# Kernel tuning notes

Hardware: AMD Instinct MI355X
Metric: run time of the kernel (lower is better)

Reference implementation:

```python
import jax, jax.numpy as jnp
import numpy as np

B, NH, N = 4, 4, 1000
NF = 256
TOPK = 10
ADJ_THRESH = 0.5
PSTEP = 3
BIG = 1e10


def construct_edges(s_cur, a_cur):
    """Top-k distance-based edge construction.
    s_cur: (B,N,3) positions, a_cur: (B,N) attributes; tool = a_cur > 0.5.
    Returns dense receiver/sender matrices Rr, Rs of shape (B, R=N*TOPK, N),
    padded with zero rows (equivalent to torch's contiguous packing).
    """
    b, n, _ = s_cur.shape
    tool = a_cur > 0.5  # mask is all-ones (no particle_nums)
    diff = s_cur[:, :, None, :] - s_cur[:, None, :, :]          # (B,N,N,3)
    dis = jnp.sum(diff * diff, axis=-1)                          # (B,N,N)
    # tool-tool pairs excluded (set huge distance)
    dis = jnp.where(tool[:, :, None] & tool[:, None, :], BIG, dis)
    neg_d, idx = jax.lax.top_k(-dis, TOPK)                       # smallest TOPK dists
    d = -neg_d                                                    # (B,N,TOPK)
    # edge valid if within threshold; receiver-is-tool edges zeroed
    # (connect_tools_all=False branch: adj[tool_mask_1 * mask_2] = 0)
    flag = (d < ADJ_THRESH * ADJ_THRESH) & (~tool[:, :, None])   # (B,N,TOPK)
    R = n * TOPK
    flagR = flag.reshape(b, R).astype(s_cur.dtype)
    send = idx.reshape(b, R)                                      # sender index per relation
    recv = jnp.repeat(jnp.arange(n), TOPK)                        # (R,) receiver index
    bi = jnp.arange(b)[:, None]
    ri = jnp.arange(R)[None, :]
    Rr = jnp.zeros((b, R, n), s_cur.dtype).at[bi, ri, recv[None, :]].set(flagR)
    Rs = jnp.zeros((b, R, n), s_cur.dtype).at[bi, ri, send].set(flagR)
    return Rr, Rs


def _forward(a_hist, s_hist, s_delta,
             pe_w0, pe_b0, pe_w1, pe_b1,
             re_w0, re_b0, re_w1, re_b1, re_w2, re_b2,
             rp_w, rp_b, pp_w, pp_b,
             pr_w0, pr_b0, pr_w1, pr_b1):
    relu = jax.nn.relu
    b, nh, n = a_hist.shape
    a = jnp.swapaxes(a_hist, 1, 2)                 # (B,N,NH)
    s = jnp.swapaxes(s_hist, 1, 2)                 # (B,N,NH,3)
    sd = jnp.swapaxes(s_delta, 1, 2).reshape(b, n, 3 * nh)  # (B,N,3*NH)
    a_cur = a[:, :, -1]                             # (B,N)
    s_cur = s[:, :, -1, :]                          # (B,N,3)

    Rr, Rs = construct_edges(s_cur, a_cur)          # (B,R,N)

    a_r = jnp.einsum('brn,bn->br', Rr, a_cur)[..., None]  # (B,R,1)
    a_s = jnp.einsum('brn,bn->br', Rs, a_cur)[..., None]
    s_r = jnp.einsum('brn,bnd->brd', Rr, s_cur)            # (B,R,3)
    s_s = jnp.einsum('brn,bnd->brd', Rs, s_cur)

    # particle encoder: Linear-ReLU-Linear-ReLU on cat[s_delta_flat, a_hist]
    pe_in = jnp.concatenate([sd, a], axis=2)               # (B,N,4*NH)
    particle_encode = relu(relu(pe_in @ pe_w0 + pe_b0) @ pe_w1 + pe_b1)

    re_in = jnp.concatenate([a_r, a_s, s_r - s_s], axis=2)
    h = relu(re_in @ re_w0 + re_b0)
    h = relu(h @ re_w1 + re_b1)
    relation_encode = relu(h @ re_w2 + re_b2)              # (B,R,NF)

    particle_effect = particle_encode
    for _ in range(PSTEP):
        eff_r = jnp.einsum('brn,bnd->brd', Rr, particle_effect)
        eff_s = jnp.einsum('brn,bnd->brd', Rs, particle_effect)
        effect_rel = relu(
            jnp.concatenate([relation_encode, eff_r, eff_s], axis=2) @ rp_w + rp_b)
        agg = jnp.einsum('brn,brd->bnd', Rr, effect_rel)   # Rr^T @ effect_rel
        particle_effect = relu(
            jnp.concatenate([particle_encode, agg], axis=2) @ pp_w + pp_b
            + particle_effect)

    pred = relu(particle_effect @ pr_w0 + pr_b0) @ pr_w1 + pr_b1  # (B,N,3)
    return pred + s_cur


def setup_inputs() -> dict:
    key = jax.random.key(0)
    ks = jax.random.split(key, 24)
    W = lambda k, shp: (jax.random.normal(k, shp, jnp.float32) * 0.05)
    inp = {
        'a_hist': jax.random.uniform(ks[0], (B, NH, N), jnp.float32),
        's_hist': jax.random.normal(ks[1], (B, NH, N, 3), jnp.float32),
        's_delta': jax.random.normal(ks[2], (B, NH, N, 3), jnp.float32),
        'pe_w0': W(ks[3], (4 * NH, NF)), 'pe_b0': W(ks[4], (NF,)),
        'pe_w1': W(ks[5], (NF, NF)),     'pe_b1': W(ks[6], (NF,)),
        're_w0': W(ks[7], (5, NF)),      're_b0': W(ks[8], (NF,)),
        're_w1': W(ks[9], (NF, NF)),     're_b1': W(ks[10], (NF,)),
        're_w2': W(ks[11], (NF, NF)),    're_b2': W(ks[12], (NF,)),
        'rp_w': W(ks[13], (3 * NF, NF)), 'rp_b': W(ks[14], (NF,)),
        'pp_w': W(ks[15], (2 * NF, NF)), 'pp_b': W(ks[16], (NF,)),
        'pr_w0': W(ks[17], (NF, NF)),    'pr_b0': W(ks[18], (NF,)),
        'pr_w1': W(ks[19], (NF, 3)),     'pr_b1': W(ks[20], (3,)),
    }
    return inp


def reference(a_hist, s_hist, s_delta,
              pe_w0, pe_b0, pe_w1, pe_b1,
              re_w0, re_b0, re_w1, re_b1, re_w2, re_b2,
              rp_w, rp_b, pp_w, pp_b,
              pr_w0, pr_b0, pr_w1, pr_b1):
    return _forward(a_hist, s_hist, s_delta,
                    pe_w0, pe_b0, pe_w1, pe_b1,
                    re_w0, re_b0, re_w1, re_b1, re_w2, re_b2,
                    rp_w, rp_b, pp_w, pp_b,
                    pr_w0, pr_b0, pr_w1, pr_b1)
```

## Files before the change

### kernel.cpp

```cpp
#include <hip/hip_runtime.h>
#include <hip/hip_bf16.h>

typedef unsigned short u16;
typedef unsigned int u32;

#define BATCH 4
#define NHIST 4
#define NPART 1000
#define NTOPK 10
#define NPT (BATCH*NPART)
#define NET (NPT*NTOPK)
#define EREG 5000
#define NRT 157

typedef __bf16 b8v __attribute__((ext_vector_type(8)));
typedef float  f4v __attribute__((ext_vector_type(4)));

__device__ __forceinline__ float bf2f(u16 b){
    return __uint_as_float(((u32)b) << 16);
}
__device__ __forceinline__ u16 f2bf(float f){
    u32 u = __float_as_uint(f);
    u32 r = u + 0x7FFF + ((u >> 16) & 1);
    return (u16)(r >> 16);
}
__device__ __forceinline__ float ldin(const void* p, size_t i, int isf32){
    return isf32 ? ((const float*)p)[i] : bf2f(((const u16*)p)[i]);
}

__global__ __launch_bounds__(256) void k_setup(
    const void* __restrict__ a_hist, const void* __restrict__ s_hist,
    const void* __restrict__ s_delta,
    const void* w0, const void* w1, const void* w2, const void* w3,
    const void* w4, const void* w5, const void* w6, const void* w7,
    u16* __restrict__ wsw, int* __restrict__ dflag,
    float* __restrict__ s_cur, u16* __restrict__ pe_in,
    int* __restrict__ ecount8, int* __restrict__ cidx, int* __restrict__ csend,
    u16* __restrict__ re_in)
{
    __shared__ u32 SMEM[8192];
    __shared__ int sdet;
    __shared__ int wcnt[4], wbase[4];
    int t = threadIdx.x;
    if (t == 0) sdet = 0;
    __syncthreads();
    {
        const u16* p = (const u16*)a_hist;
        int bad = 0;
        for (int i = t; i < 2000; i += 256) bad |= (p[i] >> 15) & 1;
        if (bad) atomicOr(&sdet, 1);
    }
    __syncthreads();
    int isf32 = sdet;
    int bid = blockIdx.x;

    if (bid < 74){
        const int nck[8] = {1,8,1,8,8,24,16,8};
        const int Ks[8]  = {16,256,5,256,256,768,512,256};
        const void* srcs[8] = {w0,w1,w2,w3,w4,w5,w6,w7};
        int wi = 0, c = bid;
        while (c >= nck[wi]){ c -= nck[wi]; wi++; }
        const void* src = srcs[wi];
        int K = Ks[wi];
        u16* stage = (u16*)SMEM;
        #pragma unroll 4
        for (int kk = 0; kk < 32; kk++){
            int k = c*32 + kk;
            float v = (k < K) ? ldin(src, (size_t)k*256 + t, isf32) : 0.f;
            int e = (t >> 4)*512 + ((kk >> 3)*16 + (t & 15))*8 + (kk & 7);
            stage[e] = f2bf(v);
        }
        __syncthreads();
        uint4* dstv = (uint4*)(wsw + (size_t)bid * 8192);
        const uint4* sv = (const uint4*)stage;
        dstv[t] = sv[t];
        dstv[t + 256] = sv[t + 256];
        dstv[t + 512] = sv[t + 512];
        dstv[t + 768] = sv[t + 768];
        return;
    }
    if (bid < 90){
        if (bid == 74 && t == 0) dflag[0] = isf32;
        int g = (bid - 74)*256 + t;
        if (g >= NPT) return;
        int b = g / NPART, i = g - b*NPART;
        #pragma unroll
        for (int d = 0; d < 3; d++)
            s_cur[g*3 + d] = ldin(s_hist, (size_t)((b*NHIST + NHIST-1)*NPART + i)*3 + d, isf32);
        #pragma unroll
        for (int h = 0; h < NHIST; h++){
            #pragma unroll
            for (int d = 0; d < 3; d++)
                pe_in[g*32 + h*3 + d] = f2bf(ldin(s_delta, (size_t)((b*NHIST + h)*NPART + i)*3 + d, isf32));
            pe_in[g*32 + 12 + h] = f2bf(ldin(a_hist, (b*NHIST + h)*NPART + i, isf32));
        }
        #pragma unroll
        for (int k = 16; k < 32; k++) pe_in[g*32 + k] = 0;
        return;
    }
    float* sx = (float*)SMEM;
    float* sy = sx + 1000;
    float* sz = sx + 2000;
    float* sa = sx + 3000;
    u32* raw  = SMEM + 4096;
    u32* rawa = SMEM + 4096 + 3072;
    int tb = bid - 90;
    int b = tb / 250, r0 = (tb % 250) * 4;
    int wid = t >> 6, lane = t & 63;
    {
        int sbase = (b*NHIST + NHIST-1)*NPART*3;
        int abase = (b*NHIST + NHIST-1)*NPART;
        if (isf32){
            const uint4* ps = (const uint4*)((const float*)s_hist + sbase);
            for (int i = t; i < 750; i += 256) ((uint4*)raw)[i] = ps[i];
            const uint4* pa = (const uint4*)((const float*)a_hist + abase);
            if (t < 250) ((uint4*)rawa)[t] = pa[t];
        } else {
            const uint4* ps = (const uint4*)((const u16*)s_hist + sbase);
            for (int i = t; i < 375; i += 256) ((uint4*)raw)[i] = ps[i];
            const uint4* pa = (const uint4*)((const u16*)a_hist + abase);
            if (t < 125) ((uint4*)rawa)[t] = pa[t];
        }
    }
    __syncthreads();
    for (int j = t; j < NPART; j += 256){
        float vx, vy, vz, va;
        if (isf32){
            vx = ((const float*)raw)[j*3+0]; vy = ((const float*)raw)[j*3+1];
            vz = ((const float*)raw)[j*3+2]; va = ((const float*)rawa)[j];
        } else {
            vx = bf2f(((const u16*)raw)[j*3+0]); vy = bf2f(((const u16*)raw)[j*3+1]);
            vz = bf2f(((const u16*)raw)[j*3+2]); va = bf2f(((const u16*)rawa)[j]);
        }
        sx[j] = vx; sy[j] = vy; sz[j] = vz; sa[j] = va;
    }
    __syncthreads();
    int i = r0 + wid;
    float xi = sx[i], yi = sy[i], zi = sz[i];
    float ai = sa[i];
    bool tool_i = ai > 0.5f;
    float thr = tool_i ? -1.0f : 0.25f;

    float bd[NTOPK]; int bj[NTOPK];
    #pragma unroll
    for (int k = 0; k < NTOPK; k++){ bd[k] = 3.0e38f; bj[k] = 1 << 30; }
    for (int j = lane; j < NPART; j += 64){
        float dx = xi - sx[j], dy = yi - sy[j], dz = zi - sz[j];
        float d = dx*dx + dy*dy + dz*dz;
        if (d < thr && d < bd[NTOPK-1]){
            float v = d; int vj = j;
            #pragma unroll
            for (int k = 0; k < NTOPK; k++){
                bool sw = v < bd[k];
                float tv = bd[k]; int tj = bj[k];
                if (sw){ bd[k] = v; bj[k] = vj; v = tv; vj = tj; }
            }
        }
    }
    float myd = 3.0e38f; int myj = 0;
    #pragma unroll
    for (int r = 0; r < NTOPK; r++){
        float v = bd[0]; int vj = bj[0];
        #pragma unroll
        for (int s = 32; s > 0; s >>= 1){
            float ov = __shfl_xor(v, s);
            int   oj = __shfl_xor(vj, s);
            if (ov < v || (ov == v && oj < vj)){ v = ov; vj = oj; }
        }
        if (lane == r){ myd = v; myj = vj; }
        bool owner = (bd[0] == v) && (bj[0] == vj);
        if (owner){
            #pragma unroll
            for (int k = 0; k < NTOPK-1; k++){ bd[k] = bd[k+1]; bj[k] = bj[k+1]; }
            bd[NTOPK-1] = 3.0e38f; bj[NTOPK-1] = 1 << 30;
        }
    }
    bool fl = (lane < NTOPK) && (myd < 0.25f);
    int cnt = __popcll(__ballot(fl));
    if (lane == 0) wcnt[wid] = cnt;
    __syncthreads();
    if (t == 0){
        int c0 = wcnt[0], c1 = wcnt[1], c2 = wcnt[2], c3 = wcnt[3];
        int reg = tb & 7;
        int bb = atomicAdd(&ecount8[reg], c0 + c1 + c2 + c3) + reg*EREG;
        wbase[0] = bb; wbase[1] = bb + c0; wbase[2] = bb + c0 + c1; wbase[3] = bb + c0 + c1 + c2;
    }
    __syncthreads();
    int base = wbase[wid];
    if (lane < NTOPK){
        int gp = b*NPART + i;
        int ce = fl ? base + lane : -1;
        cidx[gp*NTOPK + lane] = ce;
        if (ce >= 0){
            int j = myj;
            csend[ce] = b*NPART + j;
            u32 q0 = (u32)f2bf(ai)        | ((u32)f2bf(sa[j])      << 16);
            u32 q1 = (u32)f2bf(xi - sx[j]) | ((u32)f2bf(yi - sy[j]) << 16);
            u32 q2 = (u32)f2bf(zi - sz[j]);
            uint4 v0 = {q0, q1, q2, 0};
            uint4 zz = {0, 0, 0, 0};
            uint4* rp = (uint4*)(re_in + (size_t)ce*32);
            rp[0] = v0; rp[1] = zz; rp[2] = zz; rp[3] = zz;
        }
    }
}

__global__ __launch_bounds__(256) void k_edge(
    const u16* __restrict__ re_in, const u16* __restrict__ pe_in,
    const u16* __restrict__ W0, const u16* __restrict__ W1,
    const u16* __restrict__ W2, const u16* __restrict__ W3,
    const u16* __restrict__ PW0, const u16* __restrict__ PW1,
    const u16* __restrict__ WrpB,
    const void* __restrict__ B0, const void* __restrict__ B1,
    const void* __restrict__ B2,
    const void* __restrict__ PB0, const void* __restrict__ PB1,
    const int* __restrict__ dflag, const int* __restrict__ ecount8,
    u16* __restrict__ Eout, u16* __restrict__ penc,
    u16* __restrict__ Pr, u16* __restrict__ Ps)
{
    __shared__ u16 H1[32*256];
    __shared__ u16 H2[32*256];
    __shared__ u16 S[32*32];
    int t = threadIdx.x, lane = t & 63, wave = t >> 6;
    int wm = wave >> 1, wn = wave & 1;
    int isf32 = dflag[0];
    int l15 = lane & 15, l4 = lane >> 4;

    f4v acc[8];
    b8v af, bfA[8], bfB[8];
    auto zacc = [&](){
        #pragma unroll
        for (int j = 0; j < 8; j++) acc[j] = {0.f,0.f,0.f,0.f};
    };
    auto rdWto = [&](b8v* dst, const u16* W, int kc){
        #pragma unroll
        for (int j = 0; j < 8; j++)
            dst[j] = *(const b8v*)(W + (size_t)kc*8192 + ((wn*8 + j)*64 + lane)*8);
    };
    auto domf = [&](b8v* wf){
        #pragma unroll
        for (int j = 0; j < 8; j++)
            acc[j] = __builtin_amdgcn_mfma_f32_16x16x32_bf16(af, wf[j], acc[j], 0, 0, 0);
    };
    auto rdA = [&](const u16* Hin, int kc){
        int R = wm*16 + l15;
        int up = (kc*4 + l4) ^ (R & 31);
        af = *(const b8v*)&Hin[R*256 + up*8];
    };
    auto layer = [&](const u16* Hin, const u16* Wg){
        zacc();
        rdWto(bfA, Wg, 0);
        #pragma unroll
        for (int kc = 0; kc < 8; kc += 2){
            rdWto(bfB, Wg, kc + 1);
            rdA(Hin, kc); domf(bfA);
            if (kc + 2 < 8) rdWto(bfA, Wg, kc + 2);
            rdA(Hin, kc + 1); domf(bfB);
        }
    };
    auto epiLDS = [&](u16* Hout, const void* Wb){
        #pragma unroll
        for (int j = 0; j < 8; j++){
            int col = (wn*8 + j)*16 + l15;
            float bias = ldin(Wb, col, isf32);
            int rb = wm*16 + l4*4;
            #pragma unroll
            for (int r = 0; r < 4; r++){
                float v = acc[j][r] + bias;
                v = v > 0.f ? v : 0.f;
                int rr = rb + r;
                int up = (col >> 3) ^ (rr & 31);
                Hout[rr*256 + up*8 + (col & 7)] = f2bf(v);
            }
        }
    };
    auto stLin = [&](u16* C, int row0){
        #pragma unroll
        for (int j = 0; j < 8; j++){
            int col = (wn*8 + j)*16 + l15;
            int rb = row0 + wm*16 + l4*4;
            #pragma unroll
            for (int r = 0; r < 4; r++)
                C[(size_t)(rb + r)*256 + col] = f2bf(acc[j][r]);
        }
    };

    if (blockIdx.x >= 8*NRT){
        int row0 = (blockIdx.x - 8*NRT) * 32;
        if (t < 128){
            int row = t >> 2, q = t & 3;
            int rg = row0 + row;
            uint4 v = *(const uint4*)(pe_in + (size_t)rg*32 + q*8);
            int up = q ^ (row & 3);
            *(uint4*)&S[row*32 + up*8] = v;
        }
        __syncthreads();
        zacc();
        {
            rdWto(bfA, PW0, 0);
            int R = wm*16 + l15;
            int up = l4 ^ (R & 3);
            af = *(const b8v*)&S[R*32 + up*8];
            domf(bfA);
        }
        epiLDS(H1, PB0);
        __syncthreads();
        layer(H1, PW1);
        #pragma unroll
        for (int j = 0; j < 8; j++){
            int col = (wn*8 + j)*16 + l15;
            float bias = ldin(PB1, col, isf32);
            int rb = wm*16 + l4*4;
            #pragma unroll
            for (int r = 0; r < 4; r++){
                int rr = rb + r;
                float v = acc[j][r] + bias;
                v = v > 0.f ? v : 0.f;
                penc[(size_t)(row0 + rr)*256 + col] = f2bf(v);
                int up = (col >> 3) ^ (rr & 31);
                H2[rr*256 + up*8 + (col & 7)] = f2bf(v);
            }
        }
        __syncthreads();
        layer(H2, WrpB);                      stLin(Pr, row0);
        layer(H2, WrpB + (size_t)8*8192);     stLin(Ps, row0);
        return;
    }

    int region = blockIdx.x / NRT;
    int local  = blockIdx.x - region*NRT;
    int ec = ecount8[region];
    if (local*32 >= ec) return;
    int row0 = region*EREG + local*32;
    if (t < 128){
        int row = t >> 2, q = t & 3;
        int rg = row0 + row; if (rg >= NET) rg = NET - 1;
        uint4 v = *(const uint4*)(re_in + (size_t)rg*32 + q*8);
        int up = q ^ (row & 3);
        *(uint4*)&S[row*32 + up*8] = v;
    }
    __syncthreads();

    zacc();
    {
        rdWto(bfA, W0, 0);
        int R = wm*16 + l15;
        int up = l4 ^ (R & 3);
        af = *(const b8v*)&S[R*32 + up*8];
        domf(bfA);
    }
    epiLDS(H1, B0);
    __syncthreads();
    layer(H1, W1); epiLDS(H2, B1);
    __syncthreads();
    layer(H2, W2); epiLDS(H1, B2);
    __syncthreads();
    layer(H1, W3);
    stLin(Eout, row0);
}

__global__ void k_rpagg(const u16* __restrict__ Erel, const u16* __restrict__ Pr,
                        const u16* __restrict__ Ps,
                        const int* __restrict__ cidx, const int* __restrict__ csend,
                        const void* __restrict__ rp_b,
                        const int* __restrict__ dflag, u16* __restrict__ agg)
{
    int g = blockIdx.x, c = threadIdx.x;
    int isf32 = dflag[0];
    float bias = ldin(rp_b, c, isf32);
    float pr = bf2f(Pr[(size_t)g*256 + c]);
    float s = 0.f;
    #pragma unroll
    for (int k = 0; k < NTOPK; k++){
        int ce = cidx[g*NTOPK + k];
        if (ce >= 0){
            float v = bf2f(Erel[(size_t)ce*256 + c]) + pr
                    + bf2f(Ps[(size_t)csend[ce]*256 + c]) + bias;
            s += v > 0.f ? v : 0.f;
        }
    }
    agg[(size_t)g*256 + c] = f2bf(s);
}

template<int MODE>
__global__ __launch_bounds__(256) void k_ppfuse2(
    const u16* __restrict__ penc, const u16* __restrict__ aggB,
    const u16* __restrict__ Wpp, const void* __restrict__ Bpp,
    const u16* __restrict__ res, u16* __restrict__ peff_out,
    const u16* __restrict__ WrpB, u16* __restrict__ Pr, u16* __restrict__ Ps,
    const u16* __restrict__ Wpr0, const void* __restrict__ Bpr0,
    const void* __restrict__ w1, const void* __restrict__ b1,
    const float* __restrict__ s_cur, void* __restrict__ out,
    const int* __restrict__ dflag)
{
    constexpr int SMW = (MODE == 1) ? (512 + 4096 + 4224 + 1536 + 8) : (512 + 4096);
    __shared__ u16 SM[SMW];
    u16* a_lds = SM;
    u16* H = SM + 512;
    int t = threadIdx.x, lane = t & 63, wn = t >> 6;
    int l15 = lane & 15, l4 = lane >> 4;
    int row0 = blockIdx.x * 16;
    int isf32 = dflag[0];

    f4v acc[4];
    b8v af, bfA[4], bfB[4];
    auto zacc = [&](){
        #pragma unroll
        for (int j = 0; j < 4; j++) acc[j] = {0.f,0.f,0.f,0.f};
    };
    auto rdWto = [&](b8v* dst, const u16* W, int kc){
        #pragma unroll
        for (int j = 0; j < 4; j++)
            dst[j] = *(const b8v*)(W + (size_t)kc*8192 + ((wn*4 + j)*64 + lane)*8);
    };
    auto domf = [&](b8v* wf){
        #pragma unroll
        for (int j = 0; j < 4; j++)
            acc[j] = __builtin_amdgcn_mfma_f32_16x16x32_bf16(af, wf[j], acc[j], 0, 0, 0);
    };
    auto rdH = [&](int kc){
        int R = l15;
        int up = (kc*4 + l4) ^ R;
        af = *(const b8v*)&H[R*256 + up*8];
    };
    auto layer = [&](const u16* Wg){
        zacc();
        rdWto(bfA, Wg, 0);
        #pragma unroll
        for (int kc = 0; kc < 8; kc += 2){
            rdWto(bfB, Wg, kc + 1);
            rdH(kc); domf(bfA);
            if (kc + 2 < 8) rdWto(bfA, Wg, kc + 2);
            rdH(kc + 1); domf(bfB);
        }
    };
    auto stLin = [&](u16* C){
        #pragma unroll
        for (int j = 0; j < 4; j++){
            int col = (wn*4 + j)*16 + l15;
            int rb = row0 + l4*4;
            #pragma unroll
            for (int r = 0; r < 4; r++)
                C[(size_t)(rb + r)*256 + col] = f2bf(acc[j][r]);
        }
    };
    auto stageA = [&](int kc){
        uint4 ra;
        if (t < 64){
            int row = t >> 2, up = t & 3;
            int q = up ^ ((row >> 1) & 3);
            int rg = row0 + row;
            int kg = kc*32 + q*8;
            const u16* src = (kg < 256) ? penc + (size_t)rg*256 + kg
                                        : aggB + (size_t)rg*256 + (kg - 256);
            ra = *(const uint4*)src;
        }
        __syncthreads();
        if (t < 64) ((uint4*)a_lds)[t] = ra;
        __syncthreads();
        int R = l15;
        int up = l4 ^ ((R >> 1) & 3);
        af = *(const b8v*)&a_lds[R*32 + up*8];
    };

    zacc();
    rdWto(bfA, Wpp, 0);
    for (int kc = 0; kc < 16; kc += 2){
        stageA(kc);
        rdWto(bfB, Wpp, kc + 1);
        domf(bfA);
        stageA(kc + 1);
        if (kc + 2 < 16) rdWto(bfA, Wpp, kc + 2);
        domf(bfB);
    }
    #pragma unroll
    for (int j = 0; j < 4; j++){
        int col = (wn*4 + j)*16 + l15;
        float bias = ldin(Bpp, col, isf32);
        int rb = l4*4;
        #pragma unroll
        for (int r = 0; r < 4; r++){
            int rr = rb + r;
            int row = row0 + rr;
            float v = acc[j][r] + bias + bf2f(res[(size_t)row*256 + col]);
            v = v > 0.f ? v : 0.f;
            int up = (col >> 3) ^ rr;
            H[rr*256 + up*8 + (col & 7)] = f2bf(v);
            if (MODE == 0) peff_out[(size_t)row*256 + col] = f2bf(v);
        }
    }
    __syncthreads();
    if (MODE == 0){
        layer(WrpB);                     stLin(Pr);
        layer(WrpB + (size_t)8*8192);    stLin(Ps);
    } else {
        u16* PH = SM + 512 + 4096;
        float* sw1 = (float*)(SM + 512 + 4096 + 4224);
        float* sb1 = (float*)(SM + 512 + 4096 + 4224 + 1536);
        #pragma unroll
        for (int i = 0; i < 3; i++) sw1[t + i*256] = ldin(w1, t + i*256, isf32);
        if (t < 3) sb1[t] = ldin(b1, t, isf32);
        layer(Wpr0);
        #pragma unroll
        for (int j = 0; j < 4; j++){
            int col = (wn*4 + j)*16 + l15;
            float bias = ldin(Bpr0, col, isf32);
            int rb = l4*4;
            #pragma unroll
            for (int r = 0; r < 4; r++){
                float v = acc[j][r] + bias;
                PH[(rb + r)*264 + col] = f2bf(v > 0.f ? v : 0.f);
            }
        }
        __syncthreads();
        int row = t >> 3, dd = t & 7;
        if (t < 128 && dd < 3){
            int g = row0 + row;
            float s = sb1[dd] + s_cur[g*3 + dd];
            const u16* hr = &PH[row*264];
            #pragma unroll 8
            for (int k = 0; k < 256; k++)
                s += bf2f(hr[k]) * sw1[k*3 + dd];
            if (isf32) ((float*)out)[g*3 + dd] = s;
            else       ((u16*)out)[g*3 + dd]   = f2bf(s);
        }
    }
}

extern "C" void kernel_launch(void* const* d_in, const int* in_sizes, int n_in,
                              void* d_out, int out_size, void* d_ws, size_t ws_size,
                              hipStream_t stream) {
    const void* a_hist = d_in[0];
    const void* s_hist = d_in[1];
    const void* s_delta= d_in[2];
    const void* pe_w0 = d_in[3];  const void* pe_b0 = d_in[4];
    const void* pe_w1 = d_in[5];  const void* pe_b1 = d_in[6];
    const void* re_w0 = d_in[7];  const void* re_b0 = d_in[8];
    const void* re_w1 = d_in[9];  const void* re_b1 = d_in[10];
    const void* re_w2 = d_in[11]; const void* re_b2 = d_in[12];
    const void* rp_w  = d_in[13]; const void* rp_b  = d_in[14];
    const void* pp_w  = d_in[15]; const void* pp_b  = d_in[16];
    const void* pr_w0 = d_in[17]; const void* pr_b0 = d_in[18];
    const void* pr_w1 = d_in[19]; const void* pr_b1 = d_in[20];

    char* base = (char*)d_ws;
    size_t off = 0;
    auto alloc = [&](size_t bytes) -> char* {
        char* p = base + off;
        off += (bytes + 255) & ~(size_t)255;
        return p;
    };
    int*   dflag = (int*)  alloc(16);
    int*   ecount8 = (int*)alloc(64);
    float* s_cur = (float*)alloc(NPT*3*4);
    int*   cidx  = (int*)  alloc(NET*4);
    int*   csend = (int*)  alloc(NET*4);
    u16* pe_in = (u16*)alloc((size_t)NPT*32*2);
    u16* re_in = (u16*)alloc((size_t)NET*32*2);
    u16* penc  = (u16*)alloc((size_t)NPT*256*2);
    u16* aggB  = (u16*)alloc((size_t)NPT*256*2);
    u16* peffA = (u16*)alloc((size_t)NPT*256*2);
    u16* peffB = (u16*)alloc((size_t)NPT*256*2);
    u16* PrPs  = (u16*)alloc((size_t)2*NPT*256*2);
    u16* Erel  = (u16*)alloc((size_t)NET*256*2);
    u16* wsw   = (u16*)alloc((size_t)74*8192*2);

    u16* sw_pe0 = wsw + (size_t) 0*8192;
    u16* sw_pe1 = wsw + (size_t) 1*8192;
    u16* sw_re0 = wsw + (size_t) 9*8192;
    u16* sw_re1 = wsw + (size_t)10*8192;
    u16* sw_re2 = wsw + (size_t)18*8192;
    u16* sw_rp  = wsw + (size_t)26*8192;
    u16* sw_pp  = wsw + (size_t)50*8192;
    u16* sw_pr0 = wsw + (size_t)66*8192;

    u16* Pr = PrPs;
    u16* Ps = PrPs + (size_t)NPT*256;
    u16* sw_rpB = sw_rp + (size_t)8*8192;

    hipMemsetAsync(ecount8, 0, 32, stream);

    k_setup<<<1090, 256, 0, stream>>>(a_hist, s_hist, s_delta,
        pe_w0, pe_w1, re_w0, re_w1, re_w2, rp_w, pp_w, pr_w0,
        wsw, dflag, s_cur, pe_in, ecount8, cidx, csend, re_in);

    k_edge<<<8*NRT + 125, 256, 0, stream>>>(re_in, pe_in,
        sw_re0, sw_re1, sw_re2, sw_rp, sw_pe0, sw_pe1, sw_rpB,
        re_b0, re_b1, re_b2, pe_b0, pe_b1, dflag, ecount8, Erel, penc, Pr, Ps);

    k_rpagg<<<NPT, 256, 0, stream>>>(Erel, Pr, Ps, cidx, csend, rp_b, dflag, aggB);
    k_ppfuse2<0><<<250, 256, 0, stream>>>(penc, aggB, sw_pp, pp_b, penc, peffA,
        sw_rpB, Pr, Ps, nullptr, nullptr, nullptr, nullptr, nullptr, nullptr, dflag);
    k_rpagg<<<NPT, 256, 0, stream>>>(Erel, Pr, Ps, cidx, csend, rp_b, dflag, aggB);
    k_ppfuse2<0><<<250, 256, 0, stream>>>(penc, aggB, sw_pp, pp_b, peffA, peffB,
        sw_rpB, Pr, Ps, nullptr, nullptr, nullptr, nullptr, nullptr, nullptr, dflag);
    k_rpagg<<<NPT, 256, 0, stream>>>(Erel, Pr, Ps, cidx, csend, rp_b, dflag, aggB);
    k_ppfuse2<1><<<250, 256, 0, stream>>>(penc, aggB, sw_pp, pp_b, peffB, nullptr,
        nullptr, nullptr, nullptr, sw_pr0, pr_b0, pr_w1, pr_b1, s_cur, (void*)d_out, dflag);
}
```

Baseline: 230.9 us.

## Fuse relation aggregation into particle-propagation kernel and stage A tiles in LDS

The separate k_rpagg gather/aggregate kernel is folded into the per-step propagation kernel. Each block computes the relu-summed edge messages for its 16 particles directly into a swizzled LDS tile, alongside the penc tile. The MFMA loop then reads both from LDS instead of staging 32-column chunks through global memory with two barriers per chunk. This removes three kernel launches and the aggB round trip through HBM. Pr/Ps are double-buffered so one step's outputs do not overwrite inputs other blocks are still reading. In exchange, only 250 blocks now do the gather work that previously ran across 4000 blocks, so that phase has less parallelism.

Measured after the change: 218.6 us. -5.3%, faster.

```diff
diff --git a/kernel.cpp b/kernel.cpp
--- a/kernel.cpp
+++ b/kernel.cpp
@@ -26,6 +26,15 @@
 }
 __device__ __forceinline__ float ldin(const void* p, size_t i, int isf32){
     return isf32 ? ((const float*)p)[i] : bf2f(((const u16*)p)[i]);
+}
+__device__ __forceinline__ void unp8(uint4 v, float* d){
+    d[0]=bf2f((u16)v.x); d[1]=bf2f((u16)(v.x>>16));
+    d[2]=bf2f((u16)v.y); d[3]=bf2f((u16)(v.y>>16));
+    d[4]=bf2f((u16)v.z); d[5]=bf2f((u16)(v.z>>16));
+    d[6]=bf2f((u16)v.w); d[7]=bf2f((u16)(v.w>>16));
+}
+__device__ __forceinline__ u32 pk2(float a, float b){
+    return (u32)f2bf(a) | ((u32)f2bf(b) << 16);
 }
 
 __global__ __launch_bounds__(256) void k_setup(
@@ -359,49 +368,84 @@
     stLin(Eout, row0);
 }
 
-__global__ void k_rpagg(const u16* __restrict__ Erel, const u16* __restrict__ Pr,
-                        const u16* __restrict__ Ps,
-                        const int* __restrict__ cidx, const int* __restrict__ csend,
-                        const void* __restrict__ rp_b,
-                        const int* __restrict__ dflag, u16* __restrict__ agg)
-{
-    int g = blockIdx.x, c = threadIdx.x;
-    int isf32 = dflag[0];
-    float bias = ldin(rp_b, c, isf32);
-    float pr = bf2f(Pr[(size_t)g*256 + c]);
-    float s = 0.f;
-    #pragma unroll
-    for (int k = 0; k < NTOPK; k++){
-        int ce = cidx[g*NTOPK + k];
-        if (ce >= 0){
-            float v = bf2f(Erel[(size_t)ce*256 + c]) + pr
-                    + bf2f(Ps[(size_t)csend[ce]*256 + c]) + bias;
-            s += v > 0.f ? v : 0.f;
-        }
-    }
-    agg[(size_t)g*256 + c] = f2bf(s);
-}
-
 template<int MODE>
-__global__ __launch_bounds__(256) void k_ppfuse2(
-    const u16* __restrict__ penc, const u16* __restrict__ aggB,
+__global__ __launch_bounds__(256) void k_step(
+    const u16* __restrict__ penc,
+    const u16* __restrict__ Erel,
+    const int* __restrict__ cidx, const int* __restrict__ csend,
+    const u16* __restrict__ PrIn, const u16* __restrict__ PsIn,
+    const void* __restrict__ rp_b,
     const u16* __restrict__ Wpp, const void* __restrict__ Bpp,
     const u16* __restrict__ res, u16* __restrict__ peff_out,
-    const u16* __restrict__ WrpB, u16* __restrict__ Pr, u16* __restrict__ Ps,
+    const u16* __restrict__ WrpB, u16* __restrict__ PrOut, u16* __restrict__ PsOut,
     const u16* __restrict__ Wpr0, const void* __restrict__ Bpr0,
     const void* __restrict__ w1, const void* __restrict__ b1,
     const float* __restrict__ s_cur, void* __restrict__ out,
     const int* __restrict__ dflag)
 {
-    constexpr int SMW = (MODE == 1) ? (512 + 4096 + 4224 + 1536 + 8) : (512 + 4096);
+    constexpr int SMW = (MODE == 1) ? (12288 + 4224 + 1536 + 8) : 12288;
     __shared__ u16 SM[SMW];
-    u16* a_lds = SM;
-    u16* H = SM + 512;
+    u16* pencT = SM;
+    u16* aggT  = SM + 4096;
+    u16* H     = SM + 8192;
     int t = threadIdx.x, lane = t & 63, wn = t >> 6;
     int l15 = lane & 15, l4 = lane >> 4;
     int row0 = blockIdx.x * 16;
     int isf32 = dflag[0];
 
+    {
+        int row = t >> 4, cg = t & 15;
+        int g = row0 + row;
+        int c0 = cg * 16;
+        int u0 = (cg*2) ^ row, u1 = (cg*2 + 1) ^ row;
+
+        uint4 a0 = *(const uint4*)(penc + (size_t)g*256 + c0);
+        uint4 a1 = *(const uint4*)(penc + (size_t)g*256 + c0 + 8);
+        *(uint4*)&pencT[row*256 + u0*8] = a0;
+        *(uint4*)&pencT[row*256 + u1*8] = a1;
+
+        float prb[16];
+        #pragma unroll
+        for (int i = 0; i < 16; i++) prb[i] = ldin(rp_b, c0 + i, isf32);
+        {
+            uint4 p0 = *(const uint4*)(PrIn + (size_t)g*256 + c0);
+            uint4 p1 = *(const uint4*)(PrIn + (size_t)g*256 + c0 + 8);
+            float pv[16];
+            unp8(p0, pv); unp8(p1, pv + 8);
+            #pragma unroll
+            for (int i = 0; i < 16; i++) prb[i] += pv[i];
+        }
+        float s[16];
+        #pragma unroll
+        for (int i = 0; i < 16; i++) s[i] = 0.f;
+        #pragma unroll
+        for (int k = 0; k < NTOPK; k++){
+            int ce = cidx[g*NTOPK + k];
+            if (ce >= 0){
+                int sd = csend[ce];
+                uint4 e0 = *(const uint4*)(Erel + (size_t)ce*256 + c0);
+                uint4 e1 = *(const uint4*)(Erel + (size_t)ce*256 + c0 + 8);
+                uint4 q0 = *(const uint4*)(PsIn + (size_t)sd*256 + c0);
+                uint4 q1 = *(const uint4*)(PsIn + (size_t)sd*256 + c0 + 8);
+                float ev[16], qv[16];
+                unp8(e0, ev); unp8(e1, ev + 8);
+                unp8(q0, qv); unp8(q1, qv + 8);
+                #pragma unroll
+                for (int i = 0; i < 16; i++){
+                    float v = ev[i] + qv[i] + prb[i];
+                    s[i] += v > 0.f ? v : 0.f;
+                }
+            }
+        }
+        uint4 z0, z1;
+        z0.x = pk2(s[0],s[1]);   z0.y = pk2(s[2],s[3]);
+        z0.z = pk2(s[4],s[5]);   z0.w = pk2(s[6],s[7]);
+        z1.x = pk2(s[8],s[9]);   z1.y = pk2(s[10],s[11]);
+        z1.z = pk2(s[12],s[13]); z1.w = pk2(s[14],s[15]);
+        *(uint4*)&aggT[row*256 + u0*8] = z0;
+        *(uint4*)&aggT[row*256 + u1*8] = z1;
+    }
+
     f4v acc[4];
     b8v af, bfA[4], bfB[4];
     auto zacc = [&](){
@@ -422,6 +466,13 @@
         int R = l15;
         int up = (kc*4 + l4) ^ R;
         af = *(const b8v*)&H[R*256 + up*8];
+    };
+    auto rdA2 = [&](int kc){
+        const u16* Hsrc = (kc < 8) ? pencT : aggT;
+        int kk = kc & 7;
+        int R = l15;
+        int up = (kk*4 + l4) ^ R;
+        af = *(const b8v*)&Hsrc[R*256 + up*8];
     };
     auto layer = [&](const u16* Wg){
         zacc();
@@ -444,34 +495,17 @@
                 C[(size_t)(rb + r)*256 + col] = f2bf(acc[j][r]);
         }
     };
-    auto stageA = [&](int kc){
-        uint4 ra;
-        if (t < 64){
-            int row = t >> 2, up = t & 3;
-            int q = up ^ ((row >> 1) & 3);
-            int rg = row0 + row;
-            int kg = kc*32 + q*8;
-            const u16* src = (kg < 256) ? penc + (size_t)rg*256 + kg
-                                        : aggB + (size_t)rg*256 + (kg - 256);
-            ra = *(const uint4*)src;
-        }
-        __syncthreads();
-        if (t < 64) ((uint4*)a_lds)[t] = ra;
-        __syncthreads();
-        int R = l15;
-        int up = l4 ^ ((R >> 1) & 3);
-        af = *(const b8v*)&a_lds[R*32 + up*8];
-    };
+
+    __syncthreads();
 
     zacc();
     rdWto(bfA, Wpp, 0);
+    #pragma unroll
     for (int kc = 0; kc < 16; kc += 2){
-        stageA(kc);
         rdWto(bfB, Wpp, kc + 1);
-        domf(bfA);
-        stageA(kc + 1);
+        rdA2(kc); domf(bfA);
         if (kc + 2 < 16) rdWto(bfA, Wpp, kc + 2);
-        domf(bfB);
+        rdA2(kc + 1); domf(bfB);
     }
     #pragma unroll
     for (int j = 0; j < 4; j++){
@@ -491,12 +525,12 @@
     }
     __syncthreads();
     if (MODE == 0){
-        layer(WrpB);                     stLin(Pr);
-        layer(WrpB + (size_t)8*8192);    stLin(Ps);
+        layer(WrpB);                     stLin(PrOut);
+        layer(WrpB + (size_t)8*8192);    stLin(PsOut);
     } else {
-        u16* PH = SM + 512 + 4096;
-        float* sw1 = (float*)(SM + 512 + 4096 + 4224);
-        float* sb1 = (float*)(SM + 512 + 4096 + 4224 + 1536);
+        u16* PH = SM + 12288;
+        float* sw1 = (float*)(SM + 12288 + 4224);
+        float* sb1 = (float*)(SM + 12288 + 4224 + 1536);
         #pragma unroll
         for (int i = 0; i < 3; i++) sw1[t + i*256] = ldin(w1, t + i*256, isf32);
         if (t < 3) sb1[t] = ldin(b1, t, isf32);
@@ -558,10 +592,9 @@
     u16* pe_in = (u16*)alloc((size_t)NPT*32*2);
     u16* re_in = (u16*)alloc((size_t)NET*32*2);
     u16* penc  = (u16*)alloc((size_t)NPT*256*2);
-    u16* aggB  = (u16*)alloc((size_t)NPT*256*2);
     u16* peffA = (u16*)alloc((size_t)NPT*256*2);
     u16* peffB = (u16*)alloc((size_t)NPT*256*2);
-    u16* PrPs  = (u16*)alloc((size_t)2*NPT*256*2);
+    u16* PrPs  = (u16*)alloc((size_t)4*NPT*256*2);
     u16* Erel  = (u16*)alloc((size_t)NET*256*2);
     u16* wsw   = (u16*)alloc((size_t)74*8192*2);
 
@@ -574,8 +607,10 @@
     u16* sw_pp  = wsw + (size_t)50*8192;
     u16* sw_pr0 = wsw + (size_t)66*8192;
 
-    u16* Pr = PrPs;
-    u16* Ps = PrPs + (size_t)NPT*256;
+    u16* PrA = PrPs;
+    u16* PsA = PrPs + (size_t)NPT*256;
+    u16* PrB = PrPs + (size_t)2*NPT*256;
+    u16* PsB = PrPs + (size_t)3*NPT*256;
     u16* sw_rpB = sw_rp + (size_t)8*8192;
 
     hipMemsetAsync(ecount8, 0, 32, stream);
@@ -586,15 +621,15 @@
 
     k_edge<<<8*NRT + 125, 256, 0, stream>>>(re_in, pe_in,
         sw_re0, sw_re1, sw_re2, sw_rp, sw_pe0, sw_pe1, sw_rpB,
-        re_b0, re_b1, re_b2, pe_b0, pe_b1, dflag, ecount8, Erel, penc, Pr, Ps);
-
-    k_rpagg<<<NPT, 256, 0, stream>>>(Erel, Pr, Ps, cidx, csend, rp_b, dflag, aggB);
-    k_ppfuse2<0><<<250, 256, 0, stream>>>(penc, aggB, sw_pp, pp_b, penc, peffA,
-        sw_rpB, Pr, Ps, nullptr, nullptr, nullptr, nullptr, nullptr, nullptr, dflag);
-    k_rpagg<<<NPT, 256, 0, stream>>>(Erel, Pr, Ps, cidx, csend, rp_b, dflag, aggB);
-    k_ppfuse2<0><<<250, 256, 0, stream>>>(penc, aggB, sw_pp, pp_b, peffA, peffB,
-        sw_rpB, Pr, Ps, nullptr, nullptr, nullptr, nullptr, nullptr, nullptr, dflag);
-    k_rpagg<<<NPT, 256, 0, stream>>>(Erel, Pr, Ps, cidx, csend, rp_b, dflag, aggB);
-    k_ppfuse2<1><<<250, 256, 0, stream>>>(penc, aggB, sw_pp, pp_b, peffB, nullptr,
-        nullptr, nullptr, nullptr, sw_pr0, pr_b0, pr_w1, pr_b1, s_cur, (void*)d_out, dflag);
-}
+        re_b0, re_b1, re_b2, pe_b0, pe_b1, dflag, ecount8, Erel, penc, PrA, PsA);
+
+    k_step<0><<<250, 256, 0, stream>>>(penc, Erel, cidx, csend, PrA, PsA, rp_b,
+        sw_pp, pp_b, penc, peffA, sw_rpB, PrB, PsB,
+        nullptr, nullptr, nullptr, nullptr, nullptr, nullptr, dflag);
+    k_step<0><<<250, 256, 0, stream>>>(penc, Erel, cidx, csend, PrB, PsB, rp_b,
+        sw_pp, pp_b, peffA, peffB, sw_rpB, PrA, PsA,
+        nullptr, nullptr, nullptr, nullptr, nullptr, nullptr, dflag);
+    k_step<1><<<250, 256, 0, stream>>>(penc, Erel, cidx, csend, PrA, PsA, rp_b,
+        sw_pp, pp_b, peffB, nullptr, nullptr, nullptr, nullptr,
+        sw_pr0, pr_b0, pr_w1, pr_b1, s_cur, (void*)d_out, dflag);
+}
```
